# Kernel tuning notes

Measured on AMD Instinct MI355X. Metric: run time of the kernel, lower is better.

The kernel has to match this reference:

```python
import jax, jax.numpy as jnp
import numpy as np

B, N, C = 2, 2048, 1024
H, D = 16, 64          # num_heads, head_dim
FF = 4096              # mlp hidden = 4*C
EPS = 1e-5


def layernorm(x, g, b):
    mu = jnp.mean(x, axis=-1, keepdims=True)
    var = jnp.mean((x - mu) ** 2, axis=-1, keepdims=True)
    return (x - mu) * jax.lax.rsqrt(var + EPS) * g + b


def setup_inputs() -> dict:
    key = jax.random.key(0)
    ks = jax.random.split(key, 8)
    s = lambda d: 1.0 / np.sqrt(d)
    return {
        "x": jax.random.normal(ks[0], (B, N, C), jnp.float32),
        "ln1_g": jnp.ones((C,), jnp.float32),
        "ln1_b": jnp.zeros((C,), jnp.float32),
        "qkv_w": jax.random.normal(ks[1], (3 * C, C), jnp.float32) * s(C),
        "proj_w": jax.random.normal(ks[2], (C, C), jnp.float32) * s(C),
        "proj_b": jnp.zeros((C,), jnp.float32),
        "ln2_g": jnp.ones((C,), jnp.float32),
        "ln2_b": jnp.zeros((C,), jnp.float32),
        "w1": jax.random.normal(ks[3], (FF, C), jnp.float32) * s(C),
        "b1": jnp.zeros((FF,), jnp.float32),
        "w2": jax.random.normal(ks[4], (C, FF), jnp.float32) * s(FF),
        "b2": jnp.zeros((C,), jnp.float32),
    }


def reference(x, ln1_g, ln1_b, qkv_w, proj_w, proj_b, ln2_g, ln2_b, w1, b1, w2, b2):
    # ---- attention sub-block ----
    h = layernorm(x, ln1_g, ln1_b)                       # [B,N,C]
    qkv = h @ qkv_w.T                                    # [B,N,3C]
    qkv = qkv.reshape(B, N, 3, H, D).transpose(2, 0, 3, 1, 4)  # [3,B,H,N,D]
    q, k, v = qkv[0], qkv[1], qkv[2]
    scale = D ** -0.5
    attn = jnp.einsum("bhnd,bhmd->bhnm", q, k) * scale   # [B,H,N,N]
    attn = jax.nn.softmax(attn, axis=-1)
    ao = jnp.einsum("bhnm,bhmd->bhnd", attn, v)          # [B,H,N,D]
    ao = ao.transpose(0, 2, 1, 3).reshape(B, N, C)
    x = x + ao @ proj_w.T + proj_b
    # ---- MLP sub-block ----
    h2 = layernorm(x, ln2_g, ln2_b)
    mlp = jax.nn.gelu(h2 @ w1.T + b1, approximate=False) @ w2.T + b2
    return x + mlp
```

## Files before the change

### kernel.cpp

```cpp
#include <hip/hip_runtime.h>
#include <hip/hip_bf16.h>

typedef __hip_bfloat16 obf;
typedef __attribute__((ext_vector_type(8))) __bf16 bf16x8;
typedef __attribute__((ext_vector_type(4))) float f32x4;

#define DEVINL __device__ __forceinline__

DEVINL void gload_lds16(const void* g, void* l) {
  __builtin_amdgcn_global_load_lds((const __attribute__((address_space(1))) void*)g,
                                   (__attribute__((address_space(3))) void*)l,
                                   16, 0, 0);
}

__global__ void __launch_bounds__(256) f2b_kernel(const float* __restrict__ in,
                                                  __bf16* __restrict__ out, int n8)
{
  const int i = blockIdx.x * 256 + threadIdx.x;
  if (i >= n8) return;
  const float4 a = ((const float4*)in)[i * 2];
  const float4 b = ((const float4*)in)[i * 2 + 1];
  bf16x8 o;
  o[0] = (__bf16)a.x; o[1] = (__bf16)a.y; o[2] = (__bf16)a.z; o[3] = (__bf16)a.w;
  o[4] = (__bf16)b.x; o[5] = (__bf16)b.y; o[6] = (__bf16)b.z; o[7] = (__bf16)b.w;
  ((bf16x8*)out)[i] = o;
}

__global__ void __launch_bounds__(256) ln_kernel(const float* __restrict__ xin,
    const float* __restrict__ g, const float* __restrict__ b, obf* __restrict__ out)
{
  const int row = blockIdx.x;
  const int t = threadIdx.x;
  const int lane = t & 63, w = t >> 6;
  float4 f = ((const float4*)xin)[(size_t)row * 256 + t];
  float v[4] = { f.x, f.y, f.z, f.w };
  float s1 = v[0] + v[1] + v[2] + v[3];
  float s2 = v[0]*v[0] + v[1]*v[1] + v[2]*v[2] + v[3]*v[3];
  #pragma unroll
  for (int off = 32; off >= 1; off >>= 1) {
    s1 += __shfl_xor(s1, off);
    s2 += __shfl_xor(s2, off);
  }
  __shared__ float red[8];
  if (lane == 0) { red[w] = s1; red[4 + w] = s2; }
  __syncthreads();
  s1 = red[0] + red[1] + red[2] + red[3];
  s2 = red[4] + red[5] + red[6] + red[7];
  const float mu = s1 * (1.f / 1024.f);
  const float var = s2 * (1.f / 1024.f) - mu * mu;
  const float rs = rsqrtf(var + 1e-5f);
  const float4 gv = ((const float4*)g)[t];
  const float4 bv = ((const float4*)b)[t];
  obf* op = out + (size_t)row * 1024 + t * 4;
  op[0] = __float2bfloat16((v[0] - mu) * rs * gv.x + bv.x);
  op[1] = __float2bfloat16((v[1] - mu) * rs * gv.y + bv.y);
  op[2] = __float2bfloat16((v[2] - mu) * rs * gv.z + bv.z);
  op[3] = __float2bfloat16((v[3] - mu) * rs * gv.w + bv.w);
}

enum { EPI_NONE = 0, EPI_BIAS_RES_F32OUT = 1, EPI_BIAS_GELU = 2, EPI_BIAS_RESF32_F32OUT = 3 };

template<int EPI, int NI>
__global__ void __launch_bounds__(256, 2) gemm_bt(
    const obf* __restrict__ A, const obf* __restrict__ Bw,
    void* __restrict__ Cout, const float* __restrict__ bias,
    const void* __restrict__ resid, int M, int N, int K)
{
  __shared__ __align__(16) char As[128 * 64 * 2];
  __shared__ __align__(16) char Bs[NI * 32 * 64 * 2];
  const int tid = threadIdx.x;
  const int lane = tid & 63;
  const int w = tid >> 6, wr = w >> 1, wc = w & 1;
  const int bm = blockIdx.y * 128, bn = blockIdx.x * (NI * 32);
  const size_t lda = (size_t)K * 2;

  f32x4 acc[4][NI];
  #pragma unroll
  for (int i = 0; i < 4; i++)
    #pragma unroll
    for (int j = 0; j < NI; j++) {
      acc[i][j][0] = 0.f; acc[i][j][1] = 0.f; acc[i][j][2] = 0.f; acc[i][j][3] = 0.f;
    }

  for (int k0 = 0; k0 < K; k0 += 64) {
    #pragma unroll
    for (int i = 0; i < 4; i++) {
      const int ci = tid + 256 * i;
      const int r = ci >> 3;
      const int gb = ((ci & 7) * 16) ^ ((r & 7) << 4);
      gload_lds16((const char*)A + (size_t)(bm + r) * lda + (size_t)k0 * 2 + gb, As + ci * 16);
    }
    #pragma unroll
    for (int i = 0; i < NI; i++) {
      const int ci = tid + 256 * i;
      const int r = ci >> 3;
      const int gb = ((ci & 7) * 16) ^ ((r & 7) << 4);
      gload_lds16((const char*)Bw + (size_t)(bn + r) * lda + (size_t)k0 * 2 + gb, Bs + ci * 16);
    }
    __syncthreads();

    bf16x8 af[4][2], bfr[NI][2];
    #pragma unroll
    for (int mi = 0; mi < 4; mi++) {
      const int r = wr * 64 + mi * 16 + (lane & 15);
      #pragma unroll
      for (int ks = 0; ks < 2; ks++) {
        const int cb = ks * 64 + ((lane >> 4) * 16);
        af[mi][ks] = *(const bf16x8*)(As + r * 128 + (cb ^ ((r & 7) << 4)));
      }
    }
    #pragma unroll
    for (int ni = 0; ni < NI; ni++) {
      const int r = wc * (NI * 16) + ni * 16 + (lane & 15);
      #pragma unroll
      for (int ks = 0; ks < 2; ks++) {
        const int cb = ks * 64 + ((lane >> 4) * 16);
        bfr[ni][ks] = *(const bf16x8*)(Bs + r * 128 + (cb ^ ((r & 7) << 4)));
      }
    }
    #pragma unroll
    for (int ks = 0; ks < 2; ks++)
      #pragma unroll
      for (int mi = 0; mi < 4; mi++)
        #pragma unroll
        for (int ni = 0; ni < NI; ni++)
          acc[mi][ni] = __builtin_amdgcn_mfma_f32_16x16x32_bf16(af[mi][ks], bfr[ni][ks], acc[mi][ni], 0, 0, 0);
    __syncthreads();
  }

  #pragma unroll
  for (int mi = 0; mi < 4; mi++) {
    #pragma unroll
    for (int ni = 0; ni < NI; ni++) {
      const int col = bn + wc * (NI * 16) + ni * 16 + (lane & 15);
      float bv = 0.f;
      if (EPI != EPI_NONE) bv = bias[col];
      #pragma unroll
      for (int r = 0; r < 4; r++) {
        const int row = bm + wr * 64 + mi * 16 + ((lane >> 4) << 2) + r;
        const float vacc = acc[mi][ni][r];
        const size_t idx = (size_t)row * N + col;
        if (EPI == EPI_NONE) {
          ((obf*)Cout)[idx] = __float2bfloat16(vacc);
        } else if (EPI == EPI_BIAS_RES_F32OUT) {
          const float x0 = ((const float*)resid)[idx];
          ((float*)Cout)[idx] = vacc + bv + x0;
        } else if (EPI == EPI_BIAS_GELU) {
          const float u = vacc + bv;
          ((obf*)Cout)[idx] = __float2bfloat16(0.5f * u * (1.f + erff(u * 0.70710678118f)));
        } else {
          const float x0 = ((const float*)resid)[idx];
          ((float*)Cout)[idx] = vacc + bv + x0;
        }
      }
    }
  }
}

__global__ void __launch_bounds__(256) vtrans_kernel(const obf* __restrict__ qkv, obf* __restrict__ vt)
{
  const int bh = blockIdx.y;
  const int b = bh >> 4, h = bh & 15;
  const int n0 = blockIdx.x * 64;
  __shared__ __bf16 tile[64][72];
  const int t = threadIdx.x;
  {
    const int n = t >> 2;
    const int c0 = (t & 3) * 16;
    const __bf16* src = (const __bf16*)qkv + ((size_t)(b * 2048 + n0 + n)) * 3072 + 2048 + h * 64 + c0;
    bf16x8 u0 = *(const bf16x8*)src;
    bf16x8 u1 = *(const bf16x8*)(src + 8);
    #pragma unroll
    for (int j = 0; j < 8; j++) { tile[n][c0 + j] = u0[j]; tile[n][c0 + 8 + j] = u1[j]; }
  }
  __syncthreads();
  {
    const int d = t >> 2;
    const int c0 = (t & 3) * 16;
    bf16x8 o0, o1;
    #pragma unroll
    for (int j = 0; j < 8; j++) { o0[j] = tile[c0 + j][d]; o1[j] = tile[c0 + 8 + j][d]; }
    __bf16* dst = (__bf16*)vt + ((size_t)bh * 64 + d) * 2048 + n0 + c0;
    *(bf16x8*)dst = o0;
    *(bf16x8*)(dst + 8) = o1;
  }
}

__global__ void __launch_bounds__(512, 2) attn_kernel(
    const obf* __restrict__ qkv_, const obf* __restrict__ vt_, obf* __restrict__ ao)
{
  const __bf16* qkv = (const __bf16*)qkv_;
  const __bf16* vt  = (const __bf16*)vt_;
  const int bid = blockIdx.x;
  const int xcd = bid & 7, idx = bid >> 3;
  const int bh = xcd * 4 + (idx >> 4);
  const int q0 = (idx & 15) * 128;
  const int b = bh >> 4, h = bh & 15;
  const int tid = threadIdx.x, lane = tid & 63, w = tid >> 6;
  const int l15 = lane & 15, hi = lane >> 4;

  __shared__ __align__(16) char Ks[2][64 * 128];
  __shared__ __align__(16) char Vs[2][64 * 128];
  __shared__ __align__(16) char Ps[8 * 16 * 128];

  bf16x8 qf[2];
  {
    const int qrow = q0 + w * 16 + l15;
    #pragma unroll
    for (int ks = 0; ks < 2; ks++)
      qf[ks] = *(const bf16x8*)(qkv + ((size_t)(b * 2048 + qrow)) * 3072 + h * 64 + ks * 32 + hi * 8);
  }

  f32x4 o[4];
  #pragma unroll
  for (int j = 0; j < 4; j++) { o[j][0]=0.f; o[j][1]=0.f; o[j][2]=0.f; o[j][3]=0.f; }
  float lrow[4] = { 0.f, 0.f, 0.f, 0.f };

  const float kfac = 0.125f * 1.44269504089f;

  const int kr = tid >> 3, kc = (tid & 7) * 8;
  const int kcb = (tid & 7) * 16;
  const int kswz = kcb ^ ((kr & 7) << 4);

  bf16x8 pk, pv;
  pk = *(const bf16x8*)(qkv + ((size_t)(b * 2048 + kr)) * 3072 + 1024 + h * 64 + kc);
  pv = *(const bf16x8*)(vt + ((size_t)bh * 64 + kr) * 2048 + kc);
  *(bf16x8*)(Ks[0] + kr * 128 + kswz) = pk;
  *(bf16x8*)(Vs[0] + kr * 128 + kswz) = pv;
  __syncthreads();

  for (int kt = 0; kt < 2048; kt += 64) {
    const int cur = (kt >> 6) & 1;
    if (kt + 64 < 2048) {
      pk = *(const bf16x8*)(qkv + ((size_t)(b * 2048 + kt + 64 + kr)) * 3072 + 1024 + h * 64 + kc);
      pv = *(const bf16x8*)(vt + ((size_t)bh * 64 + kr) * 2048 + kt + 64 + kc);
    }

    f32x4 s[4];
    #pragma unroll
    for (int j = 0; j < 4; j++) { s[j][0]=0.f; s[j][1]=0.f; s[j][2]=0.f; s[j][3]=0.f; }
    #pragma unroll
    for (int ni = 0; ni < 4; ni++) {
      const int r = ni * 16 + l15;
      const bf16x8 kf0 = *(const bf16x8*)(Ks[cur] + r * 128 + ((hi * 16) ^ ((r & 7) << 4)));
      const bf16x8 kf1 = *(const bf16x8*)(Ks[cur] + r * 128 + ((64 + hi * 16) ^ ((r & 7) << 4)));
      s[ni] = __builtin_amdgcn_mfma_f32_16x16x32_bf16(qf[0], kf0, s[ni], 0, 0, 0);
      s[ni] = __builtin_amdgcn_mfma_f32_16x16x32_bf16(qf[1], kf1, s[ni], 0, 0, 0);
    }

    #pragma unroll
    for (int r = 0; r < 4; r++) {
      const int qrl = (hi << 2) + r;
      char* psrow = Ps + w * 2048 + qrl * 128;
      float psum = 0.f;
      #pragma unroll
      for (int ni = 0; ni < 4; ni++) {
        const float p = exp2f(s[ni][r] * kfac);
        psum += p;
        *(__bf16*)(psrow + (((ni * 16 + l15) * 2) ^ ((qrl & 7) << 4))) = (__bf16)p;
      }
      lrow[r] += psum;
    }

    #pragma unroll
    for (int ks = 0; ks < 2; ks++) {
      const int rr = l15;
      const bf16x8 pa = *(const bf16x8*)(Ps + w * 2048 + rr * 128 + (((ks * 32 + hi * 8) * 2) ^ ((rr & 7) << 4)));
      #pragma unroll
      for (int df = 0; df < 4; df++) {
        const int dr = df * 16 + l15;
        const int cb = (ks * 32 + hi * 8) * 2;
        const bf16x8 vb = *(const bf16x8*)(Vs[cur] + dr * 128 + (cb ^ ((dr & 7) << 4)));
        o[df] = __builtin_amdgcn_mfma_f32_16x16x32_bf16(pa, vb, o[df], 0, 0, 0);
      }
    }

    if (kt + 64 < 2048) {
      *(bf16x8*)(Ks[cur ^ 1] + kr * 128 + kswz) = pk;
      *(bf16x8*)(Vs[cur ^ 1] + kr * 128 + kswz) = pv;
    }
    __syncthreads();
  }

  #pragma unroll
  for (int r = 0; r < 4; r++) {
    lrow[r] += __shfl_xor(lrow[r], 1);
    lrow[r] += __shfl_xor(lrow[r], 2);
    lrow[r] += __shfl_xor(lrow[r], 4);
    lrow[r] += __shfl_xor(lrow[r], 8);
  }
  #pragma unroll
  for (int r = 0; r < 4; r++) {
    const float inv = 1.f / lrow[r];
    const int qrow = q0 + w * 16 + (hi << 2) + r;
    #pragma unroll
    for (int df = 0; df < 4; df++) {
      const int col = h * 64 + df * 16 + l15;
      ao[((size_t)(b * 2048 + qrow)) * 1024 + col] = __float2bfloat16(o[df][r] * inv);
    }
  }
}

extern "C" void kernel_launch(void* const* d_in, const int* in_sizes, int n_in,
                              void* d_out, int out_size, void* d_ws, size_t ws_size,
                              hipStream_t stream) {
  const float* x      = (const float*)d_in[0];
  const float* ln1_g  = (const float*)d_in[1];
  const float* ln1_b  = (const float*)d_in[2];
  const float* qkv_w  = (const float*)d_in[3];
  const float* proj_w = (const float*)d_in[4];
  const float* proj_b = (const float*)d_in[5];
  const float* ln2_g  = (const float*)d_in[6];
  const float* ln2_b  = (const float*)d_in[7];
  const float* w1     = (const float*)d_in[8];
  const float* b1     = (const float*)d_in[9];
  const float* w2     = (const float*)d_in[10];
  const float* b2     = (const float*)d_in[11];
  float* out = (float*)d_out;

  char* ws = (char*)d_ws;
  float* x2   = (float*)ws;
  obf*   h    = (obf*)(ws + (16u << 20));
  obf*   qkv  = (obf*)(ws + (24u << 20));
  obf*   ao   = (obf*)(ws + (48u << 20));
  obf*   m1   = (obf*)(ws + (24u << 20));
  __bf16* slot = (__bf16*)(ws + (56u << 20));
  __bf16* wb_w2 = (__bf16*)(ws + (16u << 20));

  const int M = 4096;

  f2b_kernel<<<(3072 * 1024 / 8 + 255) / 256, 256, 0, stream>>>(qkv_w, slot, 3072 * 1024 / 8);
  ln_kernel<<<M, 256, 0, stream>>>(x, ln1_g, ln1_b, h);
  gemm_bt<EPI_NONE, 4><<<dim3(3072 / 128, M / 128), 256, 0, stream>>>(
      h, (const obf*)slot, qkv, nullptr, nullptr, M, 3072, 1024);
  vtrans_kernel<<<dim3(32, 32), 256, 0, stream>>>(qkv, (obf*)slot);
  attn_kernel<<<512, 512, 0, stream>>>(qkv, (const obf*)slot, ao);
  f2b_kernel<<<(1024 * 1024 / 8 + 255) / 256, 256, 0, stream>>>(proj_w, slot, 1024 * 1024 / 8);
  gemm_bt<EPI_BIAS_RES_F32OUT, 2><<<dim3(1024 / 64, M / 128), 256, 0, stream>>>(
      ao, (const obf*)slot, x2, proj_b, x, M, 1024, 1024);
  ln_kernel<<<M, 256, 0, stream>>>(x2, ln2_g, ln2_b, h);
  f2b_kernel<<<(4096 * 1024 / 8 + 255) / 256, 256, 0, stream>>>(w1, slot, 4096 * 1024 / 8);
  gemm_bt<EPI_BIAS_GELU, 4><<<dim3(4096 / 128, M / 128), 256, 0, stream>>>(
      h, (const obf*)slot, m1, b1, nullptr, M, 4096, 1024);
  f2b_kernel<<<(4096 * 1024 / 8 + 255) / 256, 256, 0, stream>>>(w2, wb_w2, 4096 * 1024 / 8);
  gemm_bt<EPI_BIAS_RESF32_F32OUT, 2><<<dim3(1024 / 64, M / 128), 256, 0, stream>>>(
      m1, (const obf*)wb_w2, out, b2, x2, M, 1024, 4096);
}
```

Before: 252.3 us.

## Use a 256x256-tile, 512-thread MFMA GEMM for the FC1+GELU layer

Adds a dedicated GEMM kernel for the first MLP matmul with fused bias and exact GELU. It uses 256x256 output tiles, 8 waves that each own a 128x64 sub-tile, and double-buffered LDS filled by direct global-to-LDS loads with an XOR swizzle. The goal is more operand reuse per loaded byte and fewer, larger blocks than the previous 128x128 kernel. In exchange it needs 128 KB of LDS and many accumulator registers, so only one block fits per CU. The grid of 256 blocks is a single wave, which leaves no other block to hide barrier and load latency.

```diff
diff --git a/kernel.cpp b/kernel.cpp
--- a/kernel.cpp
+++ b/kernel.cpp
@@ -157,6 +157,81 @@
   }
 }
 
+__global__ void __launch_bounds__(512, 2) gemm256_gelu(
+    const obf* __restrict__ A, const obf* __restrict__ Bw,
+    obf* __restrict__ Cout, const float* __restrict__ bias, int M, int N, int K)
+{
+  __shared__ __align__(16) char As[2][256 * 64 * 2];
+  __shared__ __align__(16) char Bs[2][256 * 64 * 2];
+  const int tid = threadIdx.x;
+  const int lane = tid & 63;
+  const int w = tid >> 6;
+  const int wr = w >> 2, wc = w & 3;
+  const int l15 = lane & 15, hi = lane >> 4;
+  const int bm = blockIdx.y * 256, bn = blockIdx.x * 256;
+  const size_t lda = (size_t)K * 2;
+
+  f32x4 acc[8][4];
+  #pragma unroll
+  for (int i = 0; i < 8; i++)
+    #pragma unroll
+    for (int j = 0; j < 4; j++) { acc[i][j][0]=0.f; acc[i][j][1]=0.f; acc[i][j][2]=0.f; acc[i][j][3]=0.f; }
+
+  auto stage = [&](int buf, int k0) {
+    #pragma unroll
+    for (int i = 0; i < 4; i++) {
+      const int ci = tid + 512 * i;
+      const int r = ci >> 3;
+      const int gb = ((ci & 7) * 16) ^ ((r & 7) << 4);
+      gload_lds16((const char*)A + (size_t)(bm + r) * lda + (size_t)k0 * 2 + gb, As[buf] + ci * 16);
+      gload_lds16((const char*)Bw + (size_t)(bn + r) * lda + (size_t)k0 * 2 + gb, Bs[buf] + ci * 16);
+    }
+  };
+
+  stage(0, 0);
+  int cur = 0;
+  for (int k0 = 0; k0 < K; k0 += 64) {
+    __syncthreads();
+    if (k0 + 64 < K) stage(cur ^ 1, k0 + 64);
+
+    #pragma unroll
+    for (int ks = 0; ks < 2; ks++) {
+      bf16x8 af[8], bfv[4];
+      #pragma unroll
+      for (int mi = 0; mi < 8; mi++) {
+        const int r = wr * 128 + mi * 16 + l15;
+        af[mi] = *(const bf16x8*)(As[cur] + r * 128 + ((ks * 64 + hi * 16) ^ ((r & 7) << 4)));
+      }
+      #pragma unroll
+      for (int ni = 0; ni < 4; ni++) {
+        const int r = wc * 64 + ni * 16 + l15;
+        bfv[ni] = *(const bf16x8*)(Bs[cur] + r * 128 + ((ks * 64 + hi * 16) ^ ((r & 7) << 4)));
+      }
+      #pragma unroll
+      for (int mi = 0; mi < 8; mi++)
+        #pragma unroll
+        for (int ni = 0; ni < 4; ni++)
+          acc[mi][ni] = __builtin_amdgcn_mfma_f32_16x16x32_bf16(af[mi], bfv[ni], acc[mi][ni], 0, 0, 0);
+    }
+    cur ^= 1;
+  }
+
+  #pragma unroll
+  for (int mi = 0; mi < 8; mi++) {
+    #pragma unroll
+    for (int ni = 0; ni < 4; ni++) {
+      const int col = bn + wc * 64 + ni * 16 + l15;
+      const float bv = bias[col];
+      #pragma unroll
+      for (int r = 0; r < 4; r++) {
+        const int row = bm + wr * 128 + mi * 16 + (hi << 2) + r;
+        const float u = acc[mi][ni][r] + bv;
+        Cout[(size_t)row * N + col] = __float2bfloat16(0.5f * u * (1.f + erff(u * 0.70710678118f)));
+      }
+    }
+  }
+}
+
 __global__ void __launch_bounds__(256) vtrans_kernel(const obf* __restrict__ qkv, obf* __restrict__ vt)
 {
   const int bh = blockIdx.y;
@@ -340,8 +415,8 @@
       ao, (const obf*)slot, x2, proj_b, x, M, 1024, 1024);
   ln_kernel<<<M, 256, 0, stream>>>(x2, ln2_g, ln2_b, h);
   f2b_kernel<<<(4096 * 1024 / 8 + 255) / 256, 256, 0, stream>>>(w1, slot, 4096 * 1024 / 8);
-  gemm_bt<EPI_BIAS_GELU, 4><<<dim3(4096 / 128, M / 128), 256, 0, stream>>>(
-      h, (const obf*)slot, m1, b1, nullptr, M, 4096, 1024);
+  gemm256_gelu<<<dim3(4096 / 256, M / 256), 512, 0, stream>>>(
+      h, (const obf*)slot, m1, b1, M, 4096, 1024);
   f2b_kernel<<<(4096 * 1024 / 8 + 255) / 256, 256, 0, stream>>>(w2, wb_w2, 4096 * 1024 / 8);
   gemm_bt<EPI_BIAS_RESF32_F32OUT, 2><<<dim3(1024 / 64, M / 128), 256, 0, stream>>>(
       m1, (const obf*)wb_w2, out, b2, x2, M, 1024, 4096);
```

After: 262.2 us. +3.9%, slower.
